# Kernel optimization log

Measured on AMD Instinct MI355X. Metric: run time of the kernel, lower is better.

The kernel has to match this reference:

```python
import jax, jax.numpy as jnp
from jax import lax
import numpy as np

N = 4096      # batch size (P*K)
D = 1024      # embedding dim
K = 8         # instances per class


def setup_inputs() -> dict:
    key = jax.random.key(0)
    x = jax.random.normal(key, (N, D), dtype=jnp.float32)
    # metric-learning embeddings are L2-normalized, keeping sims in [-1, 1]
    inputs = x / jnp.linalg.norm(x, axis=1, keepdims=True)
    targets = (jnp.arange(N) // K).astype(jnp.int32)  # balanced PK batch, sorted by class
    return {"inputs": inputs, "targets": targets}


def reference(inputs, targets):
    n = inputs.shape[0]
    sim = inputs @ inputs.T                                   # [n, n]
    same = targets[:, None] == targets[None, :]
    eye = jnp.eye(n, dtype=bool)
    pm = (same & ~eye).astype(sim.dtype)                      # positive mask (no diagonal)
    nm = (~same).astype(sim.dtype)                            # negative mask
    pos_cnt = pm.sum(1)                                       # K-1 per row
    neg_cnt = nm.sum(1)                                       # n-K per row

    # torch computes mean/std via .data[0] -> constants w.r.t. autograd
    sg = lax.stop_gradient(sim)
    pos_mean = (sg * pm).sum(1) / pos_cnt
    pos_std = jnp.sqrt((pm * (sg - pos_mean[:, None]) ** 2).sum(1) / pos_cnt)
    neg_mean = (sg * nm).sum(1) / neg_cnt
    neg_std = jnp.sqrt((nm * (sg - neg_mean[:, None]) ** 2).sum(1) / neg_cnt)
    inter = (pos_std * pos_mean + neg_std * neg_mean) / (pos_std + neg_std)  # [n]

    # hard-negative filter: keep negatives above pos_mean - 1.5*pos_std
    keep = nm * (sg > (pos_mean - 1.5 * pos_std)[:, None]).astype(sim.dtype)
    keep_cnt = keep.sum(1)
    valid = keep_cnt >= 1.0                                   # rows with no survivors are skipped

    # log(1 + exp(x)) == softplus(x), numerically stable
    d = sim - inter[:, None]
    pos_loss = (pm * jax.nn.softplus(-2.0 * d)).sum(1) / pos_cnt
    neg_loss = 0.04 * (keep * jax.nn.softplus(50.0 * d)).sum(1) / jnp.maximum(keep_cnt, 1.0)

    loss = jnp.where(valid, pos_loss + neg_loss, 0.0).sum() / n
    prec = jnp.mean((~valid).astype(jnp.float32))
    pos_d = (sg * pm).sum() / pm.sum()
    neg_d = (sg * nm).sum() / nm.sum()
    return (loss, prec, pos_d, neg_d)
```

## Files before the change

### kernel.cpp

```cpp
#include <hip/hip_runtime.h>


#define N_ROWS 4096
#define DIM    1024
#define BM     128
#define BK     64
#define NTILE  32
#define NUT    528

typedef _Float16 half_t;
typedef __attribute__((ext_vector_type(8))) _Float16 half8;
typedef __attribute__((ext_vector_type(4))) float f32x4;
typedef __attribute__((ext_vector_type(4))) unsigned short ushort4v;

#define XH_BYTES  ((size_t)N_ROWS * DIM * 2)
#define SIM_BYTES ((size_t)N_ROWS * N_ROWS * 2)

__device__ __forceinline__ unsigned short f2h_bits(float f) {
    half_t h = (half_t)f;
    return __builtin_bit_cast(unsigned short, h);
}
__device__ __forceinline__ float h2f_bits(unsigned short u) {
    half_t h = __builtin_bit_cast(half_t, u);
    return (float)h;
}
__device__ __forceinline__ float sp_fast(float x) {
    return fmaxf(x, 0.f) + __logf(1.f + __expf(-fabsf(x)));
}
__device__ __forceinline__ float wred(float v) {
#pragma unroll
    for (int m = 1; m < 64; m <<= 1) v += __shfl_xor(v, m, 64);
    return v;
}

__global__ __launch_bounds__(256) void k_convert(const float* __restrict__ x,
                                                 unsigned short* __restrict__ xh,
                                                 float* __restrict__ accum) {
    if (blockIdx.x == 0 && threadIdx.x < 8) accum[threadIdx.x] = 0.f;
    int idx = blockIdx.x * 256 + threadIdx.x;
    const float4* x4 = reinterpret_cast<const float4*>(x);
    float4 a = x4[2 * idx];
    float4 b = x4[2 * idx + 1];
    half8 h;
    h[0] = (half_t)a.x; h[1] = (half_t)a.y; h[2] = (half_t)a.z; h[3] = (half_t)a.w;
    h[4] = (half_t)b.x; h[5] = (half_t)b.y; h[6] = (half_t)b.z; h[7] = (half_t)b.w;
    *reinterpret_cast<half8*>(xh + 8 * idx) = h;
}

__global__ __launch_bounds__(256) void k_gemm(const unsigned short* __restrict__ Xh,
                                              unsigned short* __restrict__ simh) {
    const int k0 = blockIdx.x;
    const int k  = (k0 & 7) * (NUT / 8) + (k0 >> 3);
    int r = (int)((65.0f - sqrtf(4225.0f - 8.0f * (float)k)) * 0.5f);
    while ((r + 1) * (65 - (r + 1)) / 2 <= k) ++r;
    while (r * (65 - r) / 2 > k) --r;
    const int by = r;
    const int bx = r + (k - r * (65 - r) / 2);

    __shared__ __align__(16) unsigned short As[BM * BK];
    __shared__ __align__(16) unsigned short Bs[BM * BK];
    const int t = threadIdx.x;
    const int lane = t & 63;
    const int wave = t >> 6;
    const int wr = wave >> 1, wc = wave & 1;
    const int brow = by * BM;
    const int bcol = bx * BM;

    f32x4 acc[4][4];
#pragma unroll
    for (int m = 0; m < 4; ++m)
#pragma unroll
        for (int n = 0; n < 4; ++n) acc[m][n] = (f32x4){0.f, 0.f, 0.f, 0.f};

    const char* xb = reinterpret_cast<const char*>(Xh);

    for (int kt = 0; kt < DIM / BK; ++kt) {
#pragma unroll
        for (int i = 0; i < 4; ++i) {
            int off = i * 4096 + t * 16;
            int rr  = off >> 7;
            int cb  = off & 127;
            const char* gA = xb + (size_t)(brow + rr) * (DIM * 2) + kt * (BK * 2) + cb;
            const char* gB = xb + (size_t)(bcol + rr) * (DIM * 2) + kt * (BK * 2) + cb;
            __builtin_amdgcn_global_load_lds(
                (const __attribute__((address_space(1))) void*)gA,
                (__attribute__((address_space(3))) void*)((char*)As + off), 16, 0, 0);
            __builtin_amdgcn_global_load_lds(
                (const __attribute__((address_space(1))) void*)gB,
                (__attribute__((address_space(3))) void*)((char*)Bs + off), 16, 0, 0);
        }
        __syncthreads();

#pragma unroll
        for (int kk = 0; kk < 2; ++kk) {
            half8 a[4], b[4];
            const int kf = kk * 32 + (lane >> 4) * 8;
#pragma unroll
            for (int m = 0; m < 4; ++m) {
                int row = wr * 64 + m * 16 + (lane & 15);
                a[m] = *reinterpret_cast<const half8*>(As + row * BK + kf);
            }
#pragma unroll
            for (int n = 0; n < 4; ++n) {
                int row = wc * 64 + n * 16 + (lane & 15);
                b[n] = *reinterpret_cast<const half8*>(Bs + row * BK + kf);
            }
#pragma unroll
            for (int m = 0; m < 4; ++m)
#pragma unroll
                for (int n = 0; n < 4; ++n)
                    acc[m][n] = __builtin_amdgcn_mfma_f32_16x16x32_f16(a[m], b[n], acc[m][n], 0, 0, 0);
        }
        __syncthreads();
    }

    const int fr = lane & 15, fq = lane >> 4;
#pragma unroll
    for (int m = 0; m < 4; ++m) {
#pragma unroll
        for (int n = 0; n < 4; ++n) {
            int col  = bcol + wc * 64 + n * 16 + fr;
            int row0 = brow + wr * 64 + m * 16 + fq * 4;
#pragma unroll
            for (int rr = 0; rr < 4; ++rr)
                simh[(size_t)(row0 + rr) * N_ROWS + col] = f2h_bits(acc[m][n][rr]);
            if (bx != by) {
                ushort4v p;
                p[0] = f2h_bits(acc[m][n][0]);
                p[1] = f2h_bits(acc[m][n][1]);
                p[2] = f2h_bits(acc[m][n][2]);
                p[3] = f2h_bits(acc[m][n][3]);
                *reinterpret_cast<ushort4v*>(simh + (size_t)col * N_ROWS + row0) = p;
            }
        }
    }
}

__global__ __launch_bounds__(256) void k_stats(const unsigned short* __restrict__ simh,
                                               const int* __restrict__ targets,
                                               float* __restrict__ accum) {
    __shared__ float part[4][8];
    const int t = threadIdx.x;
    const int lane = t & 63;
    const int w = t >> 6;
    const int i = blockIdx.x * 4 + w;
    const int ti = targets[i];

    const uint4* r4  = reinterpret_cast<const uint4*>(simh + (size_t)i * N_ROWS);
    const int4*  tg4 = reinterpret_cast<const int4*>(targets);

    float s[8][8];
    unsigned int mpos[8];
    float ps = 0.f, ps2 = 0.f, ns = 0.f, ns2 = 0.f, pc = 0.f, nc = 0.f;

#pragma unroll
    for (int j = 0; j < 8; ++j) {
        const int ci = j * 64 + lane;
        uint4 v  = r4[ci];
        int4 ta = tg4[2 * ci];
        int4 tb = tg4[2 * ci + 1];
        unsigned m = 0;
        m |= (ta.x == ti) ? 1u   : 0u;
        m |= (ta.y == ti) ? 2u   : 0u;
        m |= (ta.z == ti) ? 4u   : 0u;
        m |= (ta.w == ti) ? 8u   : 0u;
        m |= (tb.x == ti) ? 16u  : 0u;
        m |= (tb.y == ti) ? 32u  : 0u;
        m |= (tb.z == ti) ? 64u  : 0u;
        m |= (tb.w == ti) ? 128u : 0u;
        mpos[j] = m;
        unsigned int uw0 = v.x, uw1 = v.y, uw2 = v.z, uw3 = v.w;
        s[j][0] = h2f_bits((unsigned short)(uw0 & 0xffff));
        s[j][1] = h2f_bits((unsigned short)(uw0 >> 16));
        s[j][2] = h2f_bits((unsigned short)(uw1 & 0xffff));
        s[j][3] = h2f_bits((unsigned short)(uw1 >> 16));
        s[j][4] = h2f_bits((unsigned short)(uw2 & 0xffff));
        s[j][5] = h2f_bits((unsigned short)(uw2 >> 16));
        s[j][6] = h2f_bits((unsigned short)(uw3 & 0xffff));
        s[j][7] = h2f_bits((unsigned short)(uw3 >> 16));
        const int c0 = ci * 8;
#pragma unroll
        for (int e = 0; e < 8; ++e) {
            float sv = s[j][e];
            bool pos  = (m >> e) & 1;
            bool diag = (c0 + e) == i;
            if (pos) {
                if (!diag) { ps += sv; ps2 = fmaf(sv, sv, ps2); pc += 1.f; }
            } else {
                ns += sv; ns2 = fmaf(sv, sv, ns2); nc += 1.f;
            }
        }
    }
    ps = wred(ps); ps2 = wred(ps2); pc = wred(pc);
    ns = wred(ns); ns2 = wred(ns2); nc = wred(nc);

    float pmean = ps / pc;
    float pstd  = sqrtf(fmaxf(ps2 / pc - pmean * pmean, 0.f));
    float nmean = ns / nc;
    float nstd  = sqrtf(fmaxf(ns2 / nc - nmean * nmean, 0.f));
    float inter = (pstd * pmean + nstd * nmean) / (pstd + nstd);
    float thr   = pmean - 1.5f * pstd;

    float pl = 0.f, nl = 0.f, kc = 0.f;
#pragma unroll
    for (int j = 0; j < 8; ++j) {
        const int c0 = (j * 64 + lane) * 8;
        unsigned m = mpos[j];
#pragma unroll
        for (int e = 0; e < 8; ++e) {
            float sv = s[j][e];
            float d  = sv - inter;
            bool pos  = (m >> e) & 1;
            bool diag = (c0 + e) == i;
            if (pos) {
                if (!diag) pl += sp_fast(-2.f * d);
            } else if (sv > thr) {
                kc += 1.f;
                nl += sp_fast(50.f * d);
            }
        }
    }
    pl = wred(pl); nl = wred(nl); kc = wred(kc);

    if (lane == 0) {
        bool valid = kc >= 1.f;
        part[w][0] = valid ? (pl / pc + 0.04f * nl / fmaxf(kc, 1.f)) : 0.f;
        part[w][1] = valid ? 0.f : 1.f;
        part[w][2] = ps;
        part[w][3] = pc;
        part[w][4] = ns;
        part[w][5] = nc;
    }
    __syncthreads();
    if (t < 6) {
        float v = part[0][t] + part[1][t] + part[2][t] + part[3][t];
        atomicAdd(&accum[t], v);
    }
}

__global__ void k_final(const float* __restrict__ acc, float* __restrict__ out) {
    if (threadIdx.x == 0) {
        out[0] = acc[0] / (float)N_ROWS;
        out[1] = acc[1] / (float)N_ROWS;
        out[2] = acc[2] / acc[3];
        out[3] = acc[4] / acc[5];
    }
}

extern "C" void kernel_launch(void* const* d_in, const int* in_sizes, int n_in,
                              void* d_out, int out_size, void* d_ws, size_t ws_size,
                              hipStream_t stream) {
    const float* x       = (const float*)d_in[0];
    const int*   targets = (const int*)d_in[1];
    float*       out     = (float*)d_out;
    char*        ws      = (char*)d_ws;

    unsigned short* Xh    = (unsigned short*)ws;
    unsigned short* simh  = (unsigned short*)(ws + XH_BYTES);
    float*          accum = (float*)(ws + XH_BYTES + SIM_BYTES);

    k_convert<<<2048, 256, 0, stream>>>(x, Xh, accum);
    k_gemm<<<NUT, 256, 0, stream>>>(Xh, simh);
    k_stats<<<N_ROWS / 4, 256, 0, stream>>>(simh, targets, accum);
    k_final<<<1, 64, 0, stream>>>(accum, out);
}
```

Before: 157.9 us.

## Double-buffer GEMM LDS tiles and XOR-swizzle layout to avoid bank conflicts

The similarity GEMM now keeps two LDS buffers per operand and issues the global-to-LDS loads for the next K tile before computing on the current one, leaving one barrier per iteration instead of two. The global source column is XOR-swizzled by row so that the LDS fragment reads hit different banks. The aim is to hide global load latency and cut LDS bank conflicts. It doubles LDS use per block, which may lower occupancy.

```diff
diff --git a/kernel.cpp b/kernel.cpp
--- a/kernel.cpp
+++ b/kernel.cpp
@@ -7,6 +7,7 @@
 #define BK     64
 #define NTILE  32
 #define NUT    528
+#define NKT    (DIM / BK)
 
 typedef _Float16 half_t;
 typedef __attribute__((ext_vector_type(8))) _Float16 half8;
@@ -57,8 +58,8 @@
     const int by = r;
     const int bx = r + (k - r * (65 - r) / 2);
 
-    __shared__ __align__(16) unsigned short As[BM * BK];
-    __shared__ __align__(16) unsigned short Bs[BM * BK];
+    __shared__ __align__(16) unsigned short As[2][BM * BK];
+    __shared__ __align__(16) unsigned short Bs[2][BM * BK];
     const int t = threadIdx.x;
     const int lane = t & 63;
     const int wave = t >> 6;
@@ -74,45 +75,66 @@
 
     const char* xb = reinterpret_cast<const char*>(Xh);
 
-    for (int kt = 0; kt < DIM / BK; ++kt) {
-#pragma unroll
-        for (int i = 0; i < 4; ++i) {
-            int off = i * 4096 + t * 16;
-            int rr  = off >> 7;
-            int cb  = off & 127;
-            const char* gA = xb + (size_t)(brow + rr) * (DIM * 2) + kt * (BK * 2) + cb;
-            const char* gB = xb + (size_t)(bcol + rr) * (DIM * 2) + kt * (BK * 2) + cb;
-            __builtin_amdgcn_global_load_lds(
-                (const __attribute__((address_space(1))) void*)gA,
-                (__attribute__((address_space(3))) void*)((char*)As + off), 16, 0, 0);
-            __builtin_amdgcn_global_load_lds(
-                (const __attribute__((address_space(1))) void*)gB,
-                (__attribute__((address_space(3))) void*)((char*)Bs + off), 16, 0, 0);
-        }
+#define STAGE(buf, kt)                                                          \
+    {                                                                           \
+        _Pragma("unroll")                                                       \
+        for (int i = 0; i < 4; ++i) {                                           \
+            int off = i * 4096 + t * 16;                                        \
+            int rr  = off >> 7;                                                 \
+            int scb = ((((off >> 4) & 7) ^ (rr & 7)) << 4);                     \
+            const char* gA = xb + (size_t)(brow + rr) * (DIM * 2) + (kt) * (BK * 2) + scb; \
+            const char* gB = xb + (size_t)(bcol + rr) * (DIM * 2) + (kt) * (BK * 2) + scb; \
+            __builtin_amdgcn_global_load_lds(                                   \
+                (const __attribute__((address_space(1))) void*)gA,              \
+                (__attribute__((address_space(3))) void*)((char*)As[buf] + off), 16, 0, 0); \
+            __builtin_amdgcn_global_load_lds(                                   \
+                (const __attribute__((address_space(1))) void*)gB,              \
+                (__attribute__((address_space(3))) void*)((char*)Bs[buf] + off), 16, 0, 0); \
+        }                                                                       \
+    }
+
+#define COMPUTE(buf)                                                            \
+    {                                                                           \
+        const char* Ab = (const char*)As[buf];                                  \
+        const char* Bb = (const char*)Bs[buf];                                  \
+        _Pragma("unroll")                                                       \
+        for (int kk = 0; kk < 2; ++kk) {                                        \
+            half8 a[4], b[4];                                                   \
+            const int kb = kk * 64 + (lane >> 4) * 16;                          \
+            _Pragma("unroll")                                                   \
+            for (int m = 0; m < 4; ++m) {                                       \
+                int ra = wr * 64 + m * 16 + (lane & 15);                        \
+                a[m] = *reinterpret_cast<const half8*>(                         \
+                    Ab + (((ra << 7) + kb) ^ ((ra & 7) << 4)));                 \
+            }                                                                   \
+            _Pragma("unroll")                                                   \
+            for (int n = 0; n < 4; ++n) {                                       \
+                int rb = wc * 64 + n * 16 + (lane & 15);                        \
+                b[n] = *reinterpret_cast<const half8*>(                         \
+                    Bb + (((rb << 7) + kb) ^ ((rb & 7) << 4)));                 \
+            }                                                                   \
+            _Pragma("unroll")                                                   \
+            for (int m = 0; m < 4; ++m)                                         \
+                _Pragma("unroll")                                               \
+                for (int n = 0; n < 4; ++n)                                     \
+                    acc[m][n] = __builtin_amdgcn_mfma_f32_16x16x32_f16(         \
+                        a[m], b[n], acc[m][n], 0, 0, 0);                        \
+        }                                                                       \
+    }
+
+    STAGE(0, 0);
+    __syncthreads();
+    int cur = 0;
+    for (int kt = 0; kt < NKT - 1; ++kt) {
+        STAGE(cur ^ 1, kt + 1);
+        COMPUTE(cur);
         __syncthreads();
-
-#pragma unroll
-        for (int kk = 0; kk < 2; ++kk) {
-            half8 a[4], b[4];
-            const int kf = kk * 32 + (lane >> 4) * 8;
-#pragma unroll
-            for (int m = 0; m < 4; ++m) {
-                int row = wr * 64 + m * 16 + (lane & 15);
-                a[m] = *reinterpret_cast<const half8*>(As + row * BK + kf);
-            }
-#pragma unroll
-            for (int n = 0; n < 4; ++n) {
-                int row = wc * 64 + n * 16 + (lane & 15);
-                b[n] = *reinterpret_cast<const half8*>(Bs + row * BK + kf);
-            }
-#pragma unroll
-            for (int m = 0; m < 4; ++m)
-#pragma unroll
-                for (int n = 0; n < 4; ++n)
-                    acc[m][n] = __builtin_amdgcn_mfma_f32_16x16x32_f16(a[m], b[n], acc[m][n], 0, 0, 0);
-        }
-        __syncthreads();
-    }
+        cur ^= 1;
+    }
+    COMPUTE(cur);
+
+#undef STAGE
+#undef COMPUTE
 
     const int fr = lane & 15, fq = lane >> 4;
 #pragma unroll
```

After: 147.8 us. 1.07x faster.
